# Kernel optimization log

Hardware: AMD Instinct MI355X
Metric: run time of the kernel (lower is better)

Reference implementation:

```python
import jax, jax.numpy as jnp
from jax import lax
import numpy as np

B, C, H, W = 16, 1024, 56, 56   # batch, inplanes(=planes), spatial
G = 4                           # patch_groups
MS = 7                          # mask_size -> 8x8 pixel patches
MID = C // 4                    # planes // expansion = 256


def setup_inputs() -> dict:
    key = jax.random.key(0)
    k1, k2, k3, k4, k5 = jax.random.split(key, 5)
    x = jax.random.normal(k1, (B, C, H, W), jnp.float32)
    # binary routing mask per (batch, group, patch_row, patch_col)
    mask = jax.random.randint(k2, (B, G, MS, MS), 0, 2).astype(jnp.float32)
    # torch grouped-conv weights, layout OIHW with I = in_ch // groups
    w1 = jax.random.normal(k3, (MID, C // G, 1, 1), jnp.float32) * 0.02
    w2 = jax.random.normal(k4, (MID, MID // G, 3, 3), jnp.float32) * 0.02
    w3 = jax.random.normal(k5, (C, MID // G, 1, 1), jnp.float32) * 0.02
    return {"x": x, "mask": mask, "w1": w1, "w2": w2, "w3": w3}


def _gconv(v, w, pad, g):
    # grouped NCHW conv, stride 1, like F.conv2d(..., groups=g)
    return lax.conv_general_dilated(
        v, w, (1, 1), [(pad, pad), (pad, pad)],
        dimension_numbers=("NCHW", "OIHW", "NCHW"),
        feature_group_count=g)


def reference(x, mask, w1, w2, w3):
    b, c, h, w_ = x.shape
    g, ms = mask.shape[1], mask.shape[2]
    cpg = c // g          # channels per group
    hp = h // ms          # pixels per patch side
    # patchify: [b,c,h,w] -> [b,g,cpg,ms,hp,ms,hp] -> patches as batch dim
    # [b*ms*ms, g*cpg, hp, hp]; grouped conv applies each group's weight
    # slice to its channel slab, matching the per-group weight slicing in
    # calc_one_group. padding=1 on conv2 is PER-PATCH (zero pad at patch
    # boundary), exactly as the dispatched inference path computes it.
    xp = x.reshape(b, g, cpg, ms, hp, ms, hp)
    xp = xp.transpose(0, 3, 5, 1, 2, 4, 6).reshape(b * ms * ms, c, hp, hp)
    o = jax.nn.relu(_gconv(xp, w1, 0, g))   # 1x1
    o = jax.nn.relu(_gconv(o, w2, 1, g))    # 3x3, per-patch pad 1
    o = _gconv(o, w3, 0, g)                 # 1x1 -> c_out = planes
    cout = w3.shape[0]
    cog = cout // g
    o = o.reshape(b, ms, ms, g, cog, hp, hp)
    # zero out non-selected patches (combine/scatter step)
    m = (mask > 0).astype(o.dtype).transpose(0, 2, 3, 1)  # [b,ms,ms,g]
    o = o * m[:, :, :, :, None, None, None]
    # un-patchify back to [b, cout, h, w]
    out = o.transpose(0, 3, 4, 1, 5, 2, 6).reshape(b, cout, ms * hp, ms * hp)
    out = out + x  # residual (downsample=None, inplanes==planes)
    return jax.nn.relu(out)  # last_relu=True
```

## Files before the change

### kernel.cpp

```cpp
#include <hip/hip_runtime.h>


typedef __attribute__((ext_vector_type(8))) short bfrag;
typedef __attribute__((ext_vector_type(4))) float f4;

__device__ __forceinline__ unsigned short f2bf(float f) {
    union { float f; unsigned int i; } v; v.f = f;
    unsigned int u = v.i;
    return (unsigned short)((u + 0x7FFFu + ((u >> 16) & 1u)) >> 16);
}

__global__ __launch_bounds__(256)
void prep_weights(const float* __restrict__ w1, const float* __restrict__ w2,
                  const float* __restrict__ w3, unsigned short* __restrict__ wb) {
    int i = blockIdx.x * 256 + threadIdx.x;
    if (i < 65536) {
        wb[i] = f2bf(w1[i]);
    } else if (i < 212992) {
        int j = i - 65536;
        int ic = j & 63, ocl = (j >> 6) & 63, gt = j >> 12;
        int tap = gt % 9, g = gt / 9;
        wb[i] = f2bf(w2[(size_t)((g * 64 + ocl) * 64 + ic) * 9 + tap]);
    } else {
        wb[i] = f2bf(w3[i - 212992]);
    }
}

#define XT_S 264
#define S72  72

__global__ __launch_bounds__(256, 4)
void bottleneck_kernel(const float* __restrict__ x,
                       const float* __restrict__ mask,
                       const unsigned short* __restrict__ wbuf,
                       float* __restrict__ out) {
    __shared__ __align__(16) unsigned short lds[16896];
    unsigned short* XT = lds;
    unsigned short* Y1 = lds;
    unsigned short* Y2 = lds + 7200;

    const int tid = threadIdx.x;
    int bid = blockIdx.x;
    const int g = bid & 3;
    int p = bid >> 2;
    const int pc = p % 7; p /= 7;
    const int pr = p % 7;
    const int b  = p / 7;

    const float mval = mask[((b * 4 + g) * 7 + pr) * 7 + pc];
    const size_t xbase = (size_t)(b * 1024 + g * 256) * 3136
                       + (size_t)(pr * 8) * 56 + (size_t)(pc * 8);

    if (mval <= 0.f) {
        for (int k = 0; k < 8; k++) {
            int v = tid + k * 256;
            int ch = v >> 3, py = v & 7;
            size_t off = xbase + (size_t)ch * 3136 + (size_t)py * 56;
            float4 d0 = *(const float4*)(x + off);
            float4 d1 = *(const float4*)(x + off + 4);
            d0.x = fmaxf(d0.x, 0.f); d0.y = fmaxf(d0.y, 0.f);
            d0.z = fmaxf(d0.z, 0.f); d0.w = fmaxf(d0.w, 0.f);
            d1.x = fmaxf(d1.x, 0.f); d1.y = fmaxf(d1.y, 0.f);
            d1.z = fmaxf(d1.z, 0.f); d1.w = fmaxf(d1.w, 0.f);
            *(float4*)(out + off)     = d0;
            *(float4*)(out + off + 4) = d1;
        }
        return;
    }

    const int lane = tid & 63;
    const int wv   = tid >> 6;
    const int l15  = lane & 15;
    const int quad = lane >> 4;
    const int mrow = wv * 16 + l15;
    const int crow = wv * 16 + quad * 4;
    const int cpy  = crow >> 3, cpx0 = crow & 7;

    for (int k = 0; k < 4; k++) {
        int v = tid + k * 256;
        int py = v & 7, chp = v >> 3;
        int ch = chp * 2;
        const float* s0 = x + xbase + (size_t)ch * 3136 + (size_t)py * 56;
        const float* s1 = s0 + 3136;
        float4 a0 = *(const float4*)s0, a1 = *(const float4*)(s0 + 4);
        float4 b0 = *(const float4*)s1, b1 = *(const float4*)(s1 + 4);
        float af[8] = {a0.x,a0.y,a0.z,a0.w,a1.x,a1.y,a1.z,a1.w};
        float bg[8] = {b0.x,b0.y,b0.z,b0.w,b1.x,b1.y,b1.z,b1.w};
        int row0 = py * 8;
#pragma unroll
        for (int px = 0; px < 8; px++) {
            unsigned int u = (unsigned int)f2bf(af[px])
                           | ((unsigned int)f2bf(bg[px]) << 16);
            *(unsigned int*)&XT[(row0 + px) * XT_S + ch] = u;
        }
    }
    __syncthreads();

    const unsigned short* W1g = wbuf + (size_t)g * 16384;
    f4 acc1[4];
#pragma unroll
    for (int nt = 0; nt < 4; nt++) acc1[nt] = (f4){0.f, 0.f, 0.f, 0.f};
#pragma unroll
    for (int h = 0; h < 2; h++) {
#pragma unroll
        for (int ks = 0; ks < 4; ks++) {
            const int koff = h * 128 + ks * 32 + quad * 8;
            bfrag a = *(const bfrag*)&XT[mrow * XT_S + koff];
            bfrag b0 = *(const bfrag*)&W1g[0 * 4096 + l15 * 256 + koff];
            bfrag b1 = *(const bfrag*)&W1g[1 * 4096 + l15 * 256 + koff];
            bfrag b2 = *(const bfrag*)&W1g[2 * 4096 + l15 * 256 + koff];
            bfrag b3 = *(const bfrag*)&W1g[3 * 4096 + l15 * 256 + koff];
            __builtin_amdgcn_s_setprio(1);
            acc1[0] = __builtin_amdgcn_mfma_f32_16x16x32_bf16(a, b0, acc1[0], 0, 0, 0);
            acc1[1] = __builtin_amdgcn_mfma_f32_16x16x32_bf16(a, b1, acc1[1], 0, 0, 0);
            acc1[2] = __builtin_amdgcn_mfma_f32_16x16x32_bf16(a, b2, acc1[2], 0, 0, 0);
            acc1[3] = __builtin_amdgcn_mfma_f32_16x16x32_bf16(a, b3, acc1[3], 0, 0, 0);
            __builtin_amdgcn_s_setprio(0);
        }
    }
    __syncthreads();

    for (int i = tid; i < 36 * 72; i += 256) {
        int j = i / 72, c = i - j * 72;
        int r = (j < 10) ? j : (j < 20 ? 80 + j
                                       : 10 + ((j - 20) >> 1) * 10 + ((j - 20) & 1) * 9);
        Y1[r * S72 + c] = 0;
    }
#pragma unroll
    for (int nt = 0; nt < 4; nt++)
#pragma unroll
        for (int r = 0; r < 4; r++) {
            int px = crow + r;
            int rowp = ((px >> 3) + 1) * 10 + (px & 7) + 1;
            float v = acc1[nt][r]; v = v > 0.f ? v : 0.f;
            Y1[rowp * S72 + nt * 16 + l15] = f2bf(v);
        }
    __syncthreads();

    const unsigned short* W2g = wbuf + 65536 + (size_t)g * 36864;
    const int w2off = l15 * 64 + quad * 8;
    const int apy = mrow >> 3, apx = mrow & 7;
    f4 acc2[4];
#pragma unroll
    for (int nt = 0; nt < 4; nt++) acc2[nt] = (f4){0.f, 0.f, 0.f, 0.f};
    bfrag wA[8], wB[8];

#define LOADW2(DST, TAP) { \
    const unsigned short* tw = W2g + (TAP) * 4096 + w2off; \
    _Pragma("unroll") \
    for (int i = 0; i < 8; i++) \
        DST[i] = *(const bfrag*)&tw[(i & 3) * 1024 + (i >> 2) * 32]; }

#define TAP(T, WC, WN) { \
    if ((T) < 8) LOADW2(WN, (T) + 1); \
    const int rowp = (apy + (T) / 3) * 10 + apx + (T) % 3; \
    bfrag a0 = *(const bfrag*)&Y1[rowp * S72 + quad * 8]; \
    bfrag a1 = *(const bfrag*)&Y1[rowp * S72 + 32 + quad * 8]; \
    __builtin_amdgcn_s_setprio(1); \
    _Pragma("unroll") \
    for (int nt = 0; nt < 4; nt++) \
        acc2[nt] = __builtin_amdgcn_mfma_f32_16x16x32_bf16(a0, WC[nt], acc2[nt], 0, 0, 0); \
    _Pragma("unroll") \
    for (int nt = 0; nt < 4; nt++) \
        acc2[nt] = __builtin_amdgcn_mfma_f32_16x16x32_bf16(a1, WC[4 + nt], acc2[nt], 0, 0, 0); \
    __builtin_amdgcn_s_setprio(0); }

    LOADW2(wA, 0);
    TAP(0, wA, wB); TAP(1, wB, wA); TAP(2, wA, wB);
    TAP(3, wB, wA); TAP(4, wA, wB); TAP(5, wB, wA);
    TAP(6, wA, wB); TAP(7, wB, wA); TAP(8, wA, wB);
#undef TAP
#undef LOADW2

#pragma unroll
    for (int nt = 0; nt < 4; nt++)
#pragma unroll
        for (int r = 0; r < 4; r++) {
            int px = crow + r;
            float v = acc2[nt][r]; v = v > 0.f ? v : 0.f;
            Y2[px * S72 + nt * 16 + l15] = f2bf(v);
        }
    __syncthreads();

    const unsigned short* W3g = wbuf + 212992 + (size_t)g * 16384;
#pragma unroll
    for (int hh = 0; hh < 2; hh++) {
        f4 acc3[8];
#pragma unroll
        for (int nt = 0; nt < 8; nt++) acc3[nt] = (f4){0.f, 0.f, 0.f, 0.f};
#pragma unroll
        for (int ks = 0; ks < 2; ks++) {
            bfrag a = *(const bfrag*)&Y2[mrow * S72 + ks * 32 + quad * 8];
            __builtin_amdgcn_s_setprio(1);
#pragma unroll
            for (int nt = 0; nt < 8; nt++) {
                bfrag bb = *(const bfrag*)&W3g[(hh * 128 + nt * 16 + l15) * 64
                                               + ks * 32 + quad * 8];
                acc3[nt] = __builtin_amdgcn_mfma_f32_16x16x32_bf16(a, bb, acc3[nt], 0, 0, 0);
            }
            __builtin_amdgcn_s_setprio(0);
        }
#pragma unroll
        for (int nt = 0; nt < 8; nt++) {
            int oc = hh * 128 + nt * 16 + l15;
            size_t off = xbase + (size_t)oc * 3136 + (size_t)cpy * 56 + cpx0;
            float4 rv = *(const float4*)(x + off);
            float4 ov;
            ov.x = fmaxf(acc3[nt][0] + rv.x, 0.f);
            ov.y = fmaxf(acc3[nt][1] + rv.y, 0.f);
            ov.z = fmaxf(acc3[nt][2] + rv.z, 0.f);
            ov.w = fmaxf(acc3[nt][3] + rv.w, 0.f);
            *(float4*)(out + off) = ov;
        }
    }
}

extern "C" void kernel_launch(void* const* d_in, const int* in_sizes, int n_in,
                              void* d_out, int out_size, void* d_ws, size_t ws_size,
                              hipStream_t stream) {
    const float* x    = (const float*)d_in[0];
    const float* mask = (const float*)d_in[1];
    const float* w1   = (const float*)d_in[2];
    const float* w2   = (const float*)d_in[3];
    const float* w3   = (const float*)d_in[4];
    float* out = (float*)d_out;
    unsigned short* wbuf = (unsigned short*)d_ws;

    prep_weights<<<dim3(1088), dim3(256), 0, stream>>>(w1, w2, w3, wbuf);
    bottleneck_kernel<<<dim3(16 * 7 * 7 * 4), dim3(256), 0, stream>>>(
        x, mask, wbuf, out);
}
```

Baseline: 570.3 us.

## Stage conv weights through LDS with double-buffered 3x3 taps

The kernel stops reading MFMA B-operand weight fragments directly from global memory. All three convolutions' weights now go through LDS: w1 in two halves, w2 per tap in a double buffer with register prefetch of the next tap, and w3 in one staged copy. Residual x loads are moved ahead of the conv3 MFMAs to hide their latency. The cost is a larger LDS footprint, occupancy hint lowered from 4 to 3, and extra __syncthreads per tap.

After: 495.9 us. -13.0%, faster.

```diff
diff --git a/kernel.cpp b/kernel.cpp
--- a/kernel.cpp
+++ b/kernel.cpp
@@ -26,18 +26,25 @@
     }
 }
 
-#define XT_S 264
+#define XT_S 266
+#define W1_S 140
 #define S72  72
-
-__global__ __launch_bounds__(256, 4)
+#define W1_OFF 17024
+#define W2_OFF 7200
+#define Y2_OFF 21376
+
+__global__ __launch_bounds__(256, 3)
 void bottleneck_kernel(const float* __restrict__ x,
                        const float* __restrict__ mask,
                        const unsigned short* __restrict__ wbuf,
                        float* __restrict__ out) {
-    __shared__ __align__(16) unsigned short lds[16896];
-    unsigned short* XT = lds;
-    unsigned short* Y1 = lds;
-    unsigned short* Y2 = lds + 7200;
+    __shared__ __align__(16) unsigned short lds[25984];
+    unsigned short* XT  = lds;
+    unsigned short* Y1  = lds;
+    unsigned short* W1s = lds + W1_OFF;
+    unsigned short* W2s = lds + W2_OFF;
+    unsigned short* Y2  = lds + Y2_OFF;
+    unsigned short* W3s = lds;
 
     const int tid = threadIdx.x;
     int bid = blockIdx.x;
@@ -76,6 +83,10 @@
     const int crow = wv * 16 + quad * 4;
     const int cpy  = crow >> 3, cpx0 = crow & 7;
 
+    const unsigned short* W1g = wbuf + (size_t)g * 16384;
+    const unsigned short* W2g = wbuf + 65536 + (size_t)g * 36864;
+    const unsigned short* W3g = wbuf + 212992 + (size_t)g * 16384;
+
     for (int k = 0; k < 4; k++) {
         int v = tid + k * 256;
         int py = v & 7, chp = v >> 3;
@@ -94,29 +105,48 @@
             *(unsigned int*)&XT[(row0 + px) * XT_S + ch] = u;
         }
     }
-    __syncthreads();
-
-    const unsigned short* W1g = wbuf + (size_t)g * 16384;
+    bfrag w1n[4];
+#pragma unroll
+    for (int j = 0; j < 4; j++) {
+        int c = tid + 256 * j;
+        int oc = c >> 4, ic0 = (c & 15) << 3;
+        *(bfrag*)&W1s[oc * W1_S + ic0] = *(const bfrag*)&W1g[oc * 256 + ic0];
+        w1n[j] = *(const bfrag*)&W1g[oc * 256 + 128 + ic0];
+    }
+    __syncthreads();
+
     f4 acc1[4];
 #pragma unroll
     for (int nt = 0; nt < 4; nt++) acc1[nt] = (f4){0.f, 0.f, 0.f, 0.f};
 #pragma unroll
-    for (int h = 0; h < 2; h++) {
-#pragma unroll
-        for (int ks = 0; ks < 4; ks++) {
-            const int koff = h * 128 + ks * 32 + quad * 8;
-            bfrag a = *(const bfrag*)&XT[mrow * XT_S + koff];
-            bfrag b0 = *(const bfrag*)&W1g[0 * 4096 + l15 * 256 + koff];
-            bfrag b1 = *(const bfrag*)&W1g[1 * 4096 + l15 * 256 + koff];
-            bfrag b2 = *(const bfrag*)&W1g[2 * 4096 + l15 * 256 + koff];
-            bfrag b3 = *(const bfrag*)&W1g[3 * 4096 + l15 * 256 + koff];
-            __builtin_amdgcn_s_setprio(1);
-            acc1[0] = __builtin_amdgcn_mfma_f32_16x16x32_bf16(a, b0, acc1[0], 0, 0, 0);
-            acc1[1] = __builtin_amdgcn_mfma_f32_16x16x32_bf16(a, b1, acc1[1], 0, 0, 0);
-            acc1[2] = __builtin_amdgcn_mfma_f32_16x16x32_bf16(a, b2, acc1[2], 0, 0, 0);
-            acc1[3] = __builtin_amdgcn_mfma_f32_16x16x32_bf16(a, b3, acc1[3], 0, 0, 0);
-            __builtin_amdgcn_s_setprio(0);
-        }
+    for (int ks = 0; ks < 4; ks++) {
+        bfrag a = *(const bfrag*)&XT[mrow * XT_S + ks * 32 + quad * 8];
+        __builtin_amdgcn_s_setprio(1);
+#pragma unroll
+        for (int nt = 0; nt < 4; nt++) {
+            bfrag bb = *(const bfrag*)&W1s[(nt * 16 + l15) * W1_S + ks * 32 + quad * 8];
+            acc1[nt] = __builtin_amdgcn_mfma_f32_16x16x32_bf16(a, bb, acc1[nt], 0, 0, 0);
+        }
+        __builtin_amdgcn_s_setprio(0);
+    }
+    __syncthreads();
+#pragma unroll
+    for (int j = 0; j < 4; j++) {
+        int c = tid + 256 * j;
+        int oc = c >> 4, ic0 = (c & 15) << 3;
+        *(bfrag*)&W1s[oc * W1_S + ic0] = w1n[j];
+    }
+    __syncthreads();
+#pragma unroll
+    for (int ks = 0; ks < 4; ks++) {
+        bfrag a = *(const bfrag*)&XT[mrow * XT_S + 128 + ks * 32 + quad * 8];
+        __builtin_amdgcn_s_setprio(1);
+#pragma unroll
+        for (int nt = 0; nt < 4; nt++) {
+            bfrag bb = *(const bfrag*)&W1s[(nt * 16 + l15) * W1_S + ks * 32 + quad * 8];
+            acc1[nt] = __builtin_amdgcn_mfma_f32_16x16x32_bf16(a, bb, acc1[nt], 0, 0, 0);
+        }
+        __builtin_amdgcn_s_setprio(0);
     }
     __syncthreads();
 
@@ -135,42 +165,54 @@
             float v = acc1[nt][r]; v = v > 0.f ? v : 0.f;
             Y1[rowp * S72 + nt * 16 + l15] = f2bf(v);
         }
-    __syncthreads();
-
-    const unsigned short* W2g = wbuf + 65536 + (size_t)g * 36864;
-    const int w2off = l15 * 64 + quad * 8;
+#pragma unroll
+    for (int j = 0; j < 2; j++) {
+        int c = tid + 256 * j;
+        int oc = c >> 3, ic0 = (c & 7) << 3;
+        *(bfrag*)&W2s[oc * S72 + ic0] = *(const bfrag*)&W2g[c * 8];
+    }
+    __syncthreads();
+
+    f4 acc2[4];
+#pragma unroll
+    for (int nt = 0; nt < 4; nt++) acc2[nt] = (f4){0.f, 0.f, 0.f, 0.f};
     const int apy = mrow >> 3, apx = mrow & 7;
-    f4 acc2[4];
-#pragma unroll
-    for (int nt = 0; nt < 4; nt++) acc2[nt] = (f4){0.f, 0.f, 0.f, 0.f};
-    bfrag wA[8], wB[8];
-
-#define LOADW2(DST, TAP) { \
-    const unsigned short* tw = W2g + (TAP) * 4096 + w2off; \
-    _Pragma("unroll") \
-    for (int i = 0; i < 8; i++) \
-        DST[i] = *(const bfrag*)&tw[(i & 3) * 1024 + (i >> 2) * 32]; }
-
-#define TAP(T, WC, WN) { \
-    if ((T) < 8) LOADW2(WN, (T) + 1); \
+    bfrag wst[2];
+
+#define TAP(T) { \
+    if ((T) < 8) { \
+        _Pragma("unroll") \
+        for (int j = 0; j < 2; j++) \
+            wst[j] = *(const bfrag*)&W2g[((T) + 1) * 4096 + (tid + 256 * j) * 8]; \
+    } \
+    const int buf = ((T) & 1) * 4608; \
     const int rowp = (apy + (T) / 3) * 10 + apx + (T) % 3; \
     bfrag a0 = *(const bfrag*)&Y1[rowp * S72 + quad * 8]; \
     bfrag a1 = *(const bfrag*)&Y1[rowp * S72 + 32 + quad * 8]; \
     __builtin_amdgcn_s_setprio(1); \
     _Pragma("unroll") \
-    for (int nt = 0; nt < 4; nt++) \
-        acc2[nt] = __builtin_amdgcn_mfma_f32_16x16x32_bf16(a0, WC[nt], acc2[nt], 0, 0, 0); \
+    for (int nt = 0; nt < 4; nt++) { \
+        bfrag bb = *(const bfrag*)&W2s[buf + (nt * 16 + l15) * S72 + quad * 8]; \
+        acc2[nt] = __builtin_amdgcn_mfma_f32_16x16x32_bf16(a0, bb, acc2[nt], 0, 0, 0); \
+    } \
     _Pragma("unroll") \
-    for (int nt = 0; nt < 4; nt++) \
-        acc2[nt] = __builtin_amdgcn_mfma_f32_16x16x32_bf16(a1, WC[4 + nt], acc2[nt], 0, 0, 0); \
-    __builtin_amdgcn_s_setprio(0); }
-
-    LOADW2(wA, 0);
-    TAP(0, wA, wB); TAP(1, wB, wA); TAP(2, wA, wB);
-    TAP(3, wB, wA); TAP(4, wA, wB); TAP(5, wB, wA);
-    TAP(6, wA, wB); TAP(7, wB, wA); TAP(8, wA, wB);
+    for (int nt = 0; nt < 4; nt++) { \
+        bfrag bb = *(const bfrag*)&W2s[buf + (nt * 16 + l15) * S72 + 32 + quad * 8]; \
+        acc2[nt] = __builtin_amdgcn_mfma_f32_16x16x32_bf16(a1, bb, acc2[nt], 0, 0, 0); \
+    } \
+    __builtin_amdgcn_s_setprio(0); \
+    if ((T) < 8) { \
+        const int nb = 4608 - buf; \
+        _Pragma("unroll") \
+        for (int j = 0; j < 2; j++) { \
+            int c = tid + 256 * j; \
+            *(bfrag*)&W2s[nb + (c >> 3) * S72 + ((c & 7) << 3)] = wst[j]; \
+        } \
+        __syncthreads(); \
+    } }
+
+    TAP(0) TAP(1) TAP(2) TAP(3) TAP(4) TAP(5) TAP(6) TAP(7) TAP(8)
 #undef TAP
-#undef LOADW2
 
 #pragma unroll
     for (int nt = 0; nt < 4; nt++)
@@ -182,9 +224,23 @@
         }
     __syncthreads();
 
-    const unsigned short* W3g = wbuf + 212992 + (size_t)g * 16384;
+#pragma unroll
+    for (int j = 0; j < 8; j++) {
+        int c = tid + 256 * j;
+        int oc = c >> 3, ic0 = (c & 7) << 3;
+        *(bfrag*)&W3s[oc * S72 + ic0] = *(const bfrag*)&W3g[c * 8];
+    }
+    __syncthreads();
+
 #pragma unroll
     for (int hh = 0; hh < 2; hh++) {
+        float4 rv[8];
+#pragma unroll
+        for (int nt = 0; nt < 8; nt++) {
+            int oc = hh * 128 + nt * 16 + l15;
+            rv[nt] = *(const float4*)(x + xbase + (size_t)oc * 3136
+                                      + (size_t)cpy * 56 + cpx0);
+        }
         f4 acc3[8];
 #pragma unroll
         for (int nt = 0; nt < 8; nt++) acc3[nt] = (f4){0.f, 0.f, 0.f, 0.f};
@@ -194,7 +250,7 @@
             __builtin_amdgcn_s_setprio(1);
 #pragma unroll
             for (int nt = 0; nt < 8; nt++) {
-                bfrag bb = *(const bfrag*)&W3g[(hh * 128 + nt * 16 + l15) * 64
+                bfrag bb = *(const bfrag*)&W3s[(hh * 128 + nt * 16 + l15) * S72
                                                + ks * 32 + quad * 8];
                 acc3[nt] = __builtin_amdgcn_mfma_f32_16x16x32_bf16(a, bb, acc3[nt], 0, 0, 0);
             }
@@ -203,14 +259,13 @@
 #pragma unroll
         for (int nt = 0; nt < 8; nt++) {
             int oc = hh * 128 + nt * 16 + l15;
-            size_t off = xbase + (size_t)oc * 3136 + (size_t)cpy * 56 + cpx0;
-            float4 rv = *(const float4*)(x + off);
             float4 ov;
-            ov.x = fmaxf(acc3[nt][0] + rv.x, 0.f);
-            ov.y = fmaxf(acc3[nt][1] + rv.y, 0.f);
-            ov.z = fmaxf(acc3[nt][2] + rv.z, 0.f);
-            ov.w = fmaxf(acc3[nt][3] + rv.w, 0.f);
-            *(float4*)(out + off) = ov;
+            ov.x = fmaxf(acc3[nt][0] + rv[nt].x, 0.f);
+            ov.y = fmaxf(acc3[nt][1] + rv[nt].y, 0.f);
+            ov.z = fmaxf(acc3[nt][2] + rv[nt].z, 0.f);
+            ov.w = fmaxf(acc3[nt][3] + rv[nt].w, 0.f);
+            *(float4*)(out + xbase + (size_t)oc * 3136
+                       + (size_t)cpy * 56 + cpx0) = ov;
         }
     }
 }
```

## Remap blocks per XCD, pad XT stride, prefetch residual, drop redundant barrier

Applied to the files above, without the earlier changes.

Block indices are remapped so that each XCD processes whole (batch, group) slices. This should keep each group's weights and x rows local to one XCD's L2. The XT LDS row stride goes from 264 to 266 to change bank mapping for the transposed activation tile. The barrier before the third conv is removed because each wave reads only the Y2 rows it wrote itself. The residual x loads are issued before the final MFMAs so their latency overlaps the math. The odd stride breaks 16-byte alignment of the 128-bit LDS fragment reads, which may split them into narrower accesses.

After: 562.6 us. No clear change (-1.3%).

```diff
diff --git a/kernel.cpp b/kernel.cpp
--- a/kernel.cpp
+++ b/kernel.cpp
@@ -26,26 +26,31 @@
     }
 }
 
-#define XT_S 264
+#define XT_S 266
 #define S72  72
+#define Y2_OFF 7200
 
 __global__ __launch_bounds__(256, 4)
 void bottleneck_kernel(const float* __restrict__ x,
                        const float* __restrict__ mask,
                        const unsigned short* __restrict__ wbuf,
                        float* __restrict__ out) {
-    __shared__ __align__(16) unsigned short lds[16896];
+    __shared__ __align__(16) unsigned short lds[17024];
     unsigned short* XT = lds;
     unsigned short* Y1 = lds;
-    unsigned short* Y2 = lds + 7200;
+    unsigned short* Y2 = lds + Y2_OFF;
 
     const int tid = threadIdx.x;
     int bid = blockIdx.x;
-    const int g = bid & 3;
-    int p = bid >> 2;
-    const int pc = p % 7; p /= 7;
-    const int pr = p % 7;
-    const int b  = p / 7;
+    const int xcd  = bid & 7;
+    int slot = bid >> 3;
+    const int bgl  = slot / 49;
+    const int pat  = slot - bgl * 49;
+    const int bg   = bgl * 8 + xcd;
+    const int b    = bg >> 2;
+    const int g    = bg & 3;
+    const int pr   = pat / 7;
+    const int pc   = pat - pr * 7;
 
     const float mval = mask[((b * 4 + g) * 7 + pr) * 7 + pc];
     const size_t xbase = (size_t)(b * 1024 + g * 256) * 3136
@@ -56,14 +61,15 @@
             int v = tid + k * 256;
             int ch = v >> 3, py = v & 7;
             size_t off = xbase + (size_t)ch * 3136 + (size_t)py * 56;
-            float4 d0 = *(const float4*)(x + off);
-            float4 d1 = *(const float4*)(x + off + 4);
-            d0.x = fmaxf(d0.x, 0.f); d0.y = fmaxf(d0.y, 0.f);
-            d0.z = fmaxf(d0.z, 0.f); d0.w = fmaxf(d0.w, 0.f);
-            d1.x = fmaxf(d1.x, 0.f); d1.y = fmaxf(d1.y, 0.f);
-            d1.z = fmaxf(d1.z, 0.f); d1.w = fmaxf(d1.w, 0.f);
-            *(float4*)(out + off)     = d0;
-            *(float4*)(out + off + 4) = d1;
+            f4 d0 = *(const f4*)(x + off);
+            f4 d1 = *(const f4*)(x + off + 4);
+#pragma unroll
+            for (int e = 0; e < 4; e++) {
+                d0[e] = fmaxf(d0[e], 0.f);
+                d1[e] = fmaxf(d1[e], 0.f);
+            }
+            *(f4*)(out + off)     = d0;
+            *(f4*)(out + off + 4) = d1;
         }
         return;
     }
@@ -76,47 +82,47 @@
     const int crow = wv * 16 + quad * 4;
     const int cpy  = crow >> 3, cpx0 = crow & 7;
 
+    const unsigned short* W1g = wbuf + (size_t)g * 16384;
+    const unsigned short* W2g = wbuf + 65536 + (size_t)g * 36864;
+    const unsigned short* W3g = wbuf + 212992 + (size_t)g * 16384;
+
     for (int k = 0; k < 4; k++) {
         int v = tid + k * 256;
         int py = v & 7, chp = v >> 3;
         int ch = chp * 2;
         const float* s0 = x + xbase + (size_t)ch * 3136 + (size_t)py * 56;
         const float* s1 = s0 + 3136;
-        float4 a0 = *(const float4*)s0, a1 = *(const float4*)(s0 + 4);
-        float4 b0 = *(const float4*)s1, b1 = *(const float4*)(s1 + 4);
-        float af[8] = {a0.x,a0.y,a0.z,a0.w,a1.x,a1.y,a1.z,a1.w};
-        float bg[8] = {b0.x,b0.y,b0.z,b0.w,b1.x,b1.y,b1.z,b1.w};
+        f4 a0 = *(const f4*)s0, a1 = *(const f4*)(s0 + 4);
+        f4 b0 = *(const f4*)s1, b1 = *(const f4*)(s1 + 4);
+        float af[8] = {a0[0],a0[1],a0[2],a0[3],a1[0],a1[1],a1[2],a1[3]};
+        float bg2[8] = {b0[0],b0[1],b0[2],b0[3],b1[0],b1[1],b1[2],b1[3]};
         int row0 = py * 8;
 #pragma unroll
         for (int px = 0; px < 8; px++) {
             unsigned int u = (unsigned int)f2bf(af[px])
-                           | ((unsigned int)f2bf(bg[px]) << 16);
+                           | ((unsigned int)f2bf(bg2[px]) << 16);
             *(unsigned int*)&XT[(row0 + px) * XT_S + ch] = u;
         }
     }
     __syncthreads();
 
-    const unsigned short* W1g = wbuf + (size_t)g * 16384;
     f4 acc1[4];
 #pragma unroll
     for (int nt = 0; nt < 4; nt++) acc1[nt] = (f4){0.f, 0.f, 0.f, 0.f};
 #pragma unroll
-    for (int h = 0; h < 2; h++) {
-#pragma unroll
-        for (int ks = 0; ks < 4; ks++) {
-            const int koff = h * 128 + ks * 32 + quad * 8;
-            bfrag a = *(const bfrag*)&XT[mrow * XT_S + koff];
-            bfrag b0 = *(const bfrag*)&W1g[0 * 4096 + l15 * 256 + koff];
-            bfrag b1 = *(const bfrag*)&W1g[1 * 4096 + l15 * 256 + koff];
-            bfrag b2 = *(const bfrag*)&W1g[2 * 4096 + l15 * 256 + koff];
-            bfrag b3 = *(const bfrag*)&W1g[3 * 4096 + l15 * 256 + koff];
-            __builtin_amdgcn_s_setprio(1);
-            acc1[0] = __builtin_amdgcn_mfma_f32_16x16x32_bf16(a, b0, acc1[0], 0, 0, 0);
-            acc1[1] = __builtin_amdgcn_mfma_f32_16x16x32_bf16(a, b1, acc1[1], 0, 0, 0);
-            acc1[2] = __builtin_amdgcn_mfma_f32_16x16x32_bf16(a, b2, acc1[2], 0, 0, 0);
-            acc1[3] = __builtin_amdgcn_mfma_f32_16x16x32_bf16(a, b3, acc1[3], 0, 0, 0);
-            __builtin_amdgcn_s_setprio(0);
-        }
+    for (int kk = 0; kk < 8; kk++) {
+        const int koff = kk * 32 + quad * 8;
+        bfrag a  = *(const bfrag*)&XT[mrow * XT_S + koff];
+        bfrag b0 = *(const bfrag*)&W1g[(0 * 16 + l15) * 256 + koff];
+        bfrag b1 = *(const bfrag*)&W1g[(1 * 16 + l15) * 256 + koff];
+        bfrag b2 = *(const bfrag*)&W1g[(2 * 16 + l15) * 256 + koff];
+        bfrag b3 = *(const bfrag*)&W1g[(3 * 16 + l15) * 256 + koff];
+        __builtin_amdgcn_s_setprio(1);
+        acc1[0] = __builtin_amdgcn_mfma_f32_16x16x32_bf16(a, b0, acc1[0], 0, 0, 0);
+        acc1[1] = __builtin_amdgcn_mfma_f32_16x16x32_bf16(a, b1, acc1[1], 0, 0, 0);
+        acc1[2] = __builtin_amdgcn_mfma_f32_16x16x32_bf16(a, b2, acc1[2], 0, 0, 0);
+        acc1[3] = __builtin_amdgcn_mfma_f32_16x16x32_bf16(a, b3, acc1[3], 0, 0, 0);
+        __builtin_amdgcn_s_setprio(0);
     }
     __syncthreads();
 
@@ -137,7 +143,6 @@
         }
     __syncthreads();
 
-    const unsigned short* W2g = wbuf + 65536 + (size_t)g * 36864;
     const int w2off = l15 * 64 + quad * 8;
     const int apy = mrow >> 3, apx = mrow & 7;
     f4 acc2[4];
@@ -180,11 +185,16 @@
             float v = acc2[nt][r]; v = v > 0.f ? v : 0.f;
             Y2[px * S72 + nt * 16 + l15] = f2bf(v);
         }
-    __syncthreads();
-
-    const unsigned short* W3g = wbuf + 212992 + (size_t)g * 16384;
+
 #pragma unroll
     for (int hh = 0; hh < 2; hh++) {
+        f4 rv[8];
+#pragma unroll
+        for (int nt = 0; nt < 8; nt++) {
+            int oc = hh * 128 + nt * 16 + l15;
+            rv[nt] = *(const f4*)(x + xbase + (size_t)oc * 3136
+                                  + (size_t)cpy * 56 + cpx0);
+        }
         f4 acc3[8];
 #pragma unroll
         for (int nt = 0; nt < 8; nt++) acc3[nt] = (f4){0.f, 0.f, 0.f, 0.f};
@@ -203,14 +213,13 @@
 #pragma unroll
         for (int nt = 0; nt < 8; nt++) {
             int oc = hh * 128 + nt * 16 + l15;
-            size_t off = xbase + (size_t)oc * 3136 + (size_t)cpy * 56 + cpx0;
-            float4 rv = *(const float4*)(x + off);
-            float4 ov;
-            ov.x = fmaxf(acc3[nt][0] + rv.x, 0.f);
-            ov.y = fmaxf(acc3[nt][1] + rv.y, 0.f);
-            ov.z = fmaxf(acc3[nt][2] + rv.z, 0.f);
-            ov.w = fmaxf(acc3[nt][3] + rv.w, 0.f);
-            *(float4*)(out + off) = ov;
+            f4 ov;
+            ov[0] = fmaxf(acc3[nt][0] + rv[nt][0], 0.f);
+            ov[1] = fmaxf(acc3[nt][1] + rv[nt][1], 0.f);
+            ov[2] = fmaxf(acc3[nt][2] + rv[nt][2], 0.f);
+            ov[3] = fmaxf(acc3[nt][3] + rv[nt][3], 0.f);
+            *(f4*)(out + xbase + (size_t)oc * 3136
+                   + (size_t)cpy * 56 + cpx0) = ov;
         }
     }
 }
```
